# Performance work log

Hardware: AMD Instinct MI355X
Metric: run time of the kernel (lower is better)

The kernel has to match this reference:

```python
import jax, jax.numpy as jnp
import numpy as np

N_NODES = 100000


def gcn_conv(x, W, b, src, dst, num_nodes):
    # PyG GCNConv: add self-loops, symmetric deg^-1/2 normalization,
    # linear transform, scatter-add aggregation at dst, then bias.
    loop = jnp.arange(num_nodes, dtype=src.dtype)
    row = jnp.concatenate([src, loop])  # message sources
    col = jnp.concatenate([dst, loop])  # message destinations
    deg = jax.ops.segment_sum(jnp.ones_like(col, dtype=x.dtype), col,
                              num_segments=num_nodes)
    dinv = jnp.where(deg > 0, jax.lax.rsqrt(deg), 0.0)
    norm = dinv[row] * dinv[col]  # [E+N]
    h = x @ W  # [N, out]
    msg = h[row] * norm[:, None]  # gather + scale, [E+N, out]
    out = jax.ops.segment_sum(msg, col, num_segments=num_nodes)  # scatter-add
    return out + b


def setup_inputs() -> dict:
    key = jax.random.key(0)
    k1, k2, k3, k4, k5, k6 = jax.random.split(key, 6)
    dim_in, dim_h = 256, 128
    E = 1600000
    x = jax.random.normal(k1, (N_NODES, dim_in), dtype=jnp.float32)
    edge_index = jax.random.randint(k2, (2, E), 0, N_NODES, dtype=jnp.int64)
    # Glorot-style init for GCNConv weights
    W1 = jax.random.normal(k3, (dim_in, dim_h), dtype=jnp.float32) * (1.0 / np.sqrt(dim_in))
    b1 = jnp.zeros((dim_h,), dtype=jnp.float32)
    W2 = jax.random.normal(k4, (dim_h, 1), dtype=jnp.float32) * (1.0 / np.sqrt(dim_h))
    b2 = jnp.zeros((1,), dtype=jnp.float32)
    return {"x": x, "edge_index": edge_index, "W1": W1, "b1": b1, "W2": W2, "b2": b2}


def reference(x, edge_index, W1, b1, W2, b2):
    src, dst = edge_index[0], edge_index[1]
    h = gcn_conv(x, W1, b1, src, dst, N_NODES)
    h = jax.nn.relu(h)
    h = gcn_conv(h, W2, b2, src, dst, N_NODES)
    return jax.nn.sigmoid(h)  # [N, 1]
```

## Files before the change

kernel.cpp:

```cpp
#include <hip/hip_runtime.h>
#include <math.h>

#define NN 100000
#define DIN 256
#define DH 128
#define GEMM_NB 1563
#define BSHIFT 9
#define BNODES 512
#define NB_BUCKET 196
#define BCAP 12288
#define PA_EDGES 8192
#define PREP_NB 64

using short8  = __attribute__((ext_vector_type(8))) short;
using float4v = __attribute__((ext_vector_type(4))) float;

static __device__ __forceinline__ unsigned short f2bf(float f) {
    unsigned u = __float_as_uint(f);
    unsigned r = u + 0x7fffu + ((u >> 16) & 1u);
    return (unsigned short)(r >> 16);
}
static __device__ __forceinline__ float bf_lo(unsigned u) { return __uint_as_float(u << 16); }
static __device__ __forceinline__ float bf_hi(unsigned u) { return __uint_as_float(u & 0xffff0000u); }

__global__ __launch_bounds__(512) void k_prep_partA(const float* __restrict__ W1,
                                                    unsigned short* __restrict__ W1p,
                                                    const int* __restrict__ src,
                                                    const int* __restrict__ dst, int E,
                                                    int* __restrict__ bucketFill,
                                                    int2* __restrict__ bucketArr) {
    __shared__ int aCnt[NB_BUCKET];
    __shared__ int aBase[NB_BUCKET];
    const int tid = threadIdx.x;

    if (blockIdx.x < PREP_NB) {
        int t = blockIdx.x * 512 + tid;
        int lane = t & 63;
        int ks   = (t >> 6) & 7;
        int nt   = (t >> 9) & 1;
        int wv   = (t >> 10) & 3;
        int n = wv * 32 + nt * 16 + (lane & 15);
        int kbase = ks * 32 + (lane >> 4) * 8;
        short8 v;
#pragma unroll
        for (int j = 0; j < 8; ++j) v[j] = (short)f2bf(W1[(kbase + j) * DH + n]);
        *(short8*)&W1p[(long long)t * 8] = v;
        return;
    }

    const int ba = blockIdx.x - PREP_NB;
    for (int i = tid; i < NB_BUCKET; i += 512) aCnt[i] = 0;
    __syncthreads();
    const int e0   = ba * PA_EDGES;
    const int eend = min(e0 + PA_EDGES, E);
    for (int e = e0 + tid; e < eend; e += 512)
        atomicAdd(&aCnt[dst[e] >> BSHIFT], 1);
    __syncthreads();
    for (int i = tid; i < NB_BUCKET; i += 512) {
        int c = aCnt[i];
        aBase[i] = c ? atomicAdd(&bucketFill[i], c) : 0;
        aCnt[i] = 0;
    }
    __syncthreads();
    for (int e = e0 + tid; e < eend; e += 512) {
        int d = dst[e];
        int b = d >> BSHIFT;
        int r = atomicAdd(&aCnt[b], 1);
        bucketArr[(long long)b * BCAP + aBase[b] + r] = make_int2(src[e], d);
    }
}

__global__ __launch_bounds__(512) void k_gemm_partB(const float* __restrict__ x,
                                                    const unsigned short* __restrict__ W1p,
                                                    unsigned short* __restrict__ hs,
                                                    const int* __restrict__ bucketFill,
                                                    const int2* __restrict__ bucketArr,
                                                    int* __restrict__ cnt,
                                                    int* __restrict__ excl,
                                                    float* __restrict__ dinv,
                                                    int* __restrict__ eidx) {
    __shared__ unsigned short aL[64 * 32 * 8];
    __shared__ int h[BNODES];
    __shared__ int hex[BNODES];
    __shared__ int st[256];
    const int tid = threadIdx.x;

    if (blockIdx.x < NB_BUCKET) {
        const int b     = blockIdx.x;
        const int nbase = b << BSHIFT;
        const int len   = bucketFill[b];
        const long long abase = (long long)b * BCAP;

        if (tid < 256) st[tid] = (tid < b) ? bucketFill[tid] : 0;
        __syncthreads();
        for (int off = 128; off > 0; off >>= 1) {
            if (tid < off) st[tid] += st[tid + off];
            __syncthreads();
        }
        const int gbase = st[0];
        __syncthreads();

        for (int i = tid; i < BNODES; i += 512) h[i] = 0;
        __syncthreads();
        for (int k = tid; k < len; k += 512)
            atomicAdd(&h[bucketArr[abase + k].y - nbase], 1);
        __syncthreads();

        int a0 = 0, a1 = 0;
        if (tid < 256) {
            a0 = h[2 * tid]; a1 = h[2 * tid + 1];
            st[tid] = a0 + a1;
        }
        __syncthreads();
        for (int off = 1; off < 256; off <<= 1) {
            int val = (tid < 256 && tid >= off) ? st[tid - off] : 0;
            __syncthreads();
            if (tid < 256) st[tid] += val;
            __syncthreads();
        }
        if (tid < 256) {
            int prev = (tid > 0) ? st[tid - 1] : 0;
            hex[2 * tid]     = prev;
            hex[2 * tid + 1] = prev + a0;
        }
        __syncthreads();

        for (int i = tid; i < BNODES; i += 512) {
            int n = nbase + i;
            if (n < NN) {
                int c = h[i];
                cnt[n]  = c;
                excl[n] = gbase + hex[i];
                dinv[n] = rsqrtf(1.0f + (float)c);
            }
        }
        for (int i = tid; i < BNODES; i += 512) h[i] = 0;
        __syncthreads();

        for (int k = tid; k < len; k += 512) {
            int2 p = bucketArr[abase + k];
            int li = p.y - nbase;
            int r = atomicAdd(&h[li], 1);
            eidx[gbase + hex[li] + r] = p.x;
        }
        return;
    }

    const int bid  = blockIdx.x - NB_BUCKET;
    const int w8   = tid >> 6;
    const int lane = tid & 63;
    const int quad = lane >> 4;
    const int m16  = lane & 15;
    const int row0 = bid * 64;

    short8 bfr[8];
#pragma unroll
    for (int ks = 0; ks < 8; ++ks)
        bfr[ks] = ((const short8*)W1p)[(w8 * 8 + ks) * 64 + lane];

#pragma unroll
    for (int it = 0; it < 4; ++it) {
        int id  = it * 512 + tid;
        int row = id >> 5;
        int kb  = id & 31;
        int gr  = row0 + row;
        float4 f0, f1;
        if (gr < NN) {
            const float* xp = &x[(long long)gr * DIN + kb * 8];
            f0 = *(const float4*)xp;
            f1 = *(const float4*)(xp + 4);
        } else {
            f0 = make_float4(0.f, 0.f, 0.f, 0.f);
            f1 = f0;
        }
        short8 v;
        v[0] = (short)f2bf(f0.x); v[1] = (short)f2bf(f0.y);
        v[2] = (short)f2bf(f0.z); v[3] = (short)f2bf(f0.w);
        v[4] = (short)f2bf(f1.x); v[5] = (short)f2bf(f1.y);
        v[6] = (short)f2bf(f1.z); v[7] = (short)f2bf(f1.w);
        int chunk = row * 32 + (kb ^ (row & 31));
        *(short8*)&aL[chunk * 8] = v;
    }
    __syncthreads();

    float4v acc[4];
#pragma unroll
    for (int mt = 0; mt < 4; ++mt) acc[mt] = (float4v)(0.0f);

#pragma unroll
    for (int mt = 0; mt < 4; ++mt) {
        int row = mt * 16 + m16;
#pragma unroll
        for (int ks = 0; ks < 8; ++ks) {
            int kb = ks * 4 + quad;
            int chunk = row * 32 + (kb ^ (row & 31));
            short8 a = *(const short8*)&aL[chunk * 8];
            acc[mt] = __builtin_amdgcn_mfma_f32_16x16x32_bf16(a, bfr[ks], acc[mt], 0, 0, 0);
        }
    }

    const int n0 = w8 * 16;
#pragma unroll
    for (int mt = 0; mt < 4; ++mt) {
#pragma unroll
        for (int r = 0; r < 4; ++r) {
            int row = row0 + mt * 16 + quad * 4 + r;
            if (row < NN)
                hs[(long long)row * DH + n0 + m16] = f2bf(acc[mt][r]);
        }
    }
}

__global__ __launch_bounds__(256) void k_agg1l2(const int* __restrict__ eidx,
                                                const int* __restrict__ excl,
                                                const int* __restrict__ cnt,
                                                const unsigned* __restrict__ hs2,
                                                const float* __restrict__ dinv,
                                                const float* __restrict__ b1,
                                                const float* __restrict__ W2,
                                                float* __restrict__ zs) {
    int w = (blockIdx.x * 256 + threadIdx.x) >> 6;
    if (w >= NN) return;
    const int lane = threadIdx.x & 63;
    const int hh   = lane >> 5;
    const int l5   = lane & 31;
    int offs = excl[w];
    int c    = cnt[w];

    float dw = dinv[w];
    const uint2* hrow = (const uint2*)hs2;

    uint2 su = hrow[(long long)w * 32 + l5];
    float ss = hh ? 0.0f : dw;
    float a0 = ss * bf_lo(su.x);
    float a1 = ss * bf_hi(su.x);
    float a2 = ss * bf_lo(su.y);
    float a3 = ss * bf_hi(su.y);

    int j = 0;
    for (; j + 7 < c; j += 8) {
        int s[4]; float es[4]; uint2 uu[4];
#pragma unroll
        for (int q = 0; q < 4; ++q) s[q] = eidx[offs + j + 2 * q + hh];
#pragma unroll
        for (int q = 0; q < 4; ++q) es[q] = dinv[s[q]];
#pragma unroll
        for (int q = 0; q < 4; ++q) uu[q] = hrow[(long long)s[q] * 32 + l5];
#pragma unroll
        for (int q = 0; q < 4; ++q) {
            a0 = fmaf(es[q], bf_lo(uu[q].x), a0);
            a1 = fmaf(es[q], bf_hi(uu[q].x), a1);
            a2 = fmaf(es[q], bf_lo(uu[q].y), a2);
            a3 = fmaf(es[q], bf_hi(uu[q].y), a3);
        }
    }
    for (; j + 1 < c; j += 2) {
        int s0 = eidx[offs + j + hh];
        float e0 = dinv[s0];
        uint2 u0 = hrow[(long long)s0 * 32 + l5];
        a0 = fmaf(e0, bf_lo(u0.x), a0);
        a1 = fmaf(e0, bf_hi(u0.x), a1);
        a2 = fmaf(e0, bf_lo(u0.y), a2);
        a3 = fmaf(e0, bf_hi(u0.y), a3);
    }
    if (j < c) {
        int s0 = eidx[offs + j];
        float e0 = hh ? 0.0f : dinv[s0];
        uint2 u0 = hrow[(long long)s0 * 32 + l5];
        a0 = fmaf(e0, bf_lo(u0.x), a0);
        a1 = fmaf(e0, bf_hi(u0.x), a1);
        a2 = fmaf(e0, bf_lo(u0.y), a2);
        a3 = fmaf(e0, bf_hi(u0.y), a3);
    }

    a0 += __shfl_xor(a0, 32);
    a1 += __shfl_xor(a1, 32);
    a2 += __shfl_xor(a2, 32);
    a3 += __shfl_xor(a3, 32);

    float4 bb = ((const float4*)b1)[l5];
    float4 ww = ((const float4*)W2)[l5];
    float r0 = fmaxf(fmaf(dw, a0, bb.x), 0.0f);
    float r1 = fmaxf(fmaf(dw, a1, bb.y), 0.0f);
    float r2 = fmaxf(fmaf(dw, a2, bb.z), 0.0f);
    float r3 = fmaxf(fmaf(dw, a3, bb.w), 0.0f);
    float v = r0 * ww.x + r1 * ww.y + r2 * ww.z + r3 * ww.w;
#pragma unroll
    for (int off = 16; off > 0; off >>= 1) v += __shfl_down(v, off);
    if (lane == 0) zs[w] = v * dw;
}

__global__ void k_agg2_final(const int* __restrict__ eidx,
                             const int* __restrict__ excl,
                             const int* __restrict__ cnt,
                             const float* __restrict__ zs,
                             const float* __restrict__ dinv,
                             const float* __restrict__ b2,
                             float* __restrict__ out) {
    int i = blockIdx.x * 256 + threadIdx.x;
    if (i >= NN) return;
    int offs = excl[i];
    int c = cnt[i];
    float v = zs[i];
    int j = 0;
    for (; j + 3 < c; j += 4) {
        int s0 = eidx[offs + j + 0];
        int s1 = eidx[offs + j + 1];
        int s2 = eidx[offs + j + 2];
        int s3 = eidx[offs + j + 3];
        v += zs[s0] + zs[s1] + zs[s2] + zs[s3];
    }
    for (; j < c; ++j) v += zs[eidx[offs + j]];
    float z = fmaf(dinv[i], v, b2[0]);
    out[i] = 1.0f / (1.0f + __expf(-z));
}

extern "C" void kernel_launch(void* const* d_in, const int* in_sizes, int n_in,
                              void* d_out, int out_size, void* d_ws, size_t ws_size,
                              hipStream_t stream) {
    const float* x  = (const float*)d_in[0];
    const int*   ei = (const int*)d_in[1];
    const float* W1 = (const float*)d_in[2];
    const float* b1 = (const float*)d_in[3];
    const float* W2 = (const float*)d_in[4];
    const float* b2 = (const float*)d_in[5];
    float* out = (float*)d_out;

    const int E = in_sizes[1] / 2;
    const int* src = ei;
    const int* dst = ei + E;

    int* wsi = (int*)d_ws;
    float* dinv       = (float*)wsi;
    int*   cnt        = wsi + NN;
    int*   excl       = cnt + NN;
    float* zs         = (float*)(excl + NN);
    int*   bucketFill = (int*)(zs + NN);
    unsigned short* W1p = (unsigned short*)(bucketFill + 256);
    int*   eidx       = (int*)(W1p + 32768);
    int2*  bucketArr  = (int2*)(eidx + E);
    unsigned short* hs = (unsigned short*)(bucketArr + (long long)NB_BUCKET * BCAP);

    const int nb_nodes = (NN + 255) / 256;
    const int pa_nb = (E + PA_EDGES - 1) / PA_EDGES;

    hipMemsetAsync(bucketFill, 0, NB_BUCKET * sizeof(int), stream);

    k_prep_partA<<<PREP_NB + pa_nb, 512, 0, stream>>>(W1, W1p, src, dst, E,
                                                      bucketFill, bucketArr);
    k_gemm_partB<<<NB_BUCKET + GEMM_NB, 512, 0, stream>>>(x, W1p, hs, bucketFill, bucketArr,
                                                          cnt, excl, dinv, eidx);

    k_agg1l2<<<(NN * 64 + 255) / 256, 256, 0, stream>>>(eidx, excl, cnt,
                                                        (const unsigned*)hs, dinv, b1, W2, zs);

    k_agg2_final<<<nb_nodes, 256, 0, stream>>>(eidx, excl, cnt, zs, dinv, b2, out);
}
```

Measured before the change: 288.2 us.

## Replace bucketed CSR build with global atomic count, scan, and scatter

Drops the two-level bucket sort, which wrote int2 pairs into per-bucket arrays and then re-sorted them locally. CSR is now built from a global atomic degree count, a 4-block prefix scan fused into the GEMM launch, and a separate scatter kernel that uses global atomics on per-node cursors. Nontemporal loads are added for x, dst/src and eidx. The aim is to cut intermediate memory traffic, at the cost of heavy global atomic contention, a serial per-thread scan segment, and one extra kernel launch.

After: 519.9 us. +80.4%, slower.

```diff
diff --git a/kernel.cpp b/kernel.cpp
--- a/kernel.cpp
+++ b/kernel.cpp
@@ -5,12 +5,10 @@
 #define DIN 256
 #define DH 128
 #define GEMM_NB 1563
-#define BSHIFT 9
-#define BNODES 512
-#define NB_BUCKET 196
-#define BCAP 12288
-#define PA_EDGES 8192
 #define PREP_NB 64
+#define CNT_NB 448
+#define SCAN_NB 4
+#define SCAN_CHUNK 25000
 
 using short8  = __attribute__((ext_vector_type(8))) short;
 using float4v = __attribute__((ext_vector_type(4))) float;
@@ -23,14 +21,10 @@
 static __device__ __forceinline__ float bf_lo(unsigned u) { return __uint_as_float(u << 16); }
 static __device__ __forceinline__ float bf_hi(unsigned u) { return __uint_as_float(u & 0xffff0000u); }
 
-__global__ __launch_bounds__(512) void k_prep_partA(const float* __restrict__ W1,
+__global__ __launch_bounds__(512) void k_prep_count(const float* __restrict__ W1,
                                                     unsigned short* __restrict__ W1p,
-                                                    const int* __restrict__ src,
                                                     const int* __restrict__ dst, int E,
-                                                    int* __restrict__ bucketFill,
-                                                    int2* __restrict__ bucketArr) {
-    __shared__ int aCnt[NB_BUCKET];
-    __shared__ int aBase[NB_BUCKET];
+                                                    int* __restrict__ cnt) {
     const int tid = threadIdx.x;
 
     if (blockIdx.x < PREP_NB) {
@@ -48,105 +42,67 @@
         return;
     }
 
-    const int ba = blockIdx.x - PREP_NB;
-    for (int i = tid; i < NB_BUCKET; i += 512) aCnt[i] = 0;
-    __syncthreads();
-    const int e0   = ba * PA_EDGES;
-    const int eend = min(e0 + PA_EDGES, E);
-    for (int e = e0 + tid; e < eend; e += 512)
-        atomicAdd(&aCnt[dst[e] >> BSHIFT], 1);
-    __syncthreads();
-    for (int i = tid; i < NB_BUCKET; i += 512) {
-        int c = aCnt[i];
-        aBase[i] = c ? atomicAdd(&bucketFill[i], c) : 0;
-        aCnt[i] = 0;
-    }
-    __syncthreads();
-    for (int e = e0 + tid; e < eend; e += 512) {
-        int d = dst[e];
-        int b = d >> BSHIFT;
-        int r = atomicAdd(&aCnt[b], 1);
-        bucketArr[(long long)b * BCAP + aBase[b] + r] = make_int2(src[e], d);
-    }
-}
-
-__global__ __launch_bounds__(512) void k_gemm_partB(const float* __restrict__ x,
-                                                    const unsigned short* __restrict__ W1p,
-                                                    unsigned short* __restrict__ hs,
-                                                    const int* __restrict__ bucketFill,
-                                                    const int2* __restrict__ bucketArr,
-                                                    int* __restrict__ cnt,
-                                                    int* __restrict__ excl,
-                                                    float* __restrict__ dinv,
-                                                    int* __restrict__ eidx) {
+    const int stride = CNT_NB * 512;
+    for (int e = (blockIdx.x - PREP_NB) * 512 + tid; e < E; e += stride) {
+        int d = __builtin_nontemporal_load(&dst[e]);
+        atomicAdd(&cnt[d], 1);
+    }
+}
+
+__global__ __launch_bounds__(512) void k_gemm_scan(const float* __restrict__ x,
+                                                   const unsigned short* __restrict__ W1p,
+                                                   unsigned short* __restrict__ hs,
+                                                   const int* __restrict__ cnt,
+                                                   int* __restrict__ excl,
+                                                   int* __restrict__ cur,
+                                                   float* __restrict__ dinv) {
     __shared__ unsigned short aL[64 * 32 * 8];
-    __shared__ int h[BNODES];
-    __shared__ int hex[BNODES];
-    __shared__ int st[256];
     const int tid = threadIdx.x;
 
-    if (blockIdx.x < NB_BUCKET) {
-        const int b     = blockIdx.x;
-        const int nbase = b << BSHIFT;
-        const int len   = bucketFill[b];
-        const long long abase = (long long)b * BCAP;
-
-        if (tid < 256) st[tid] = (tid < b) ? bucketFill[tid] : 0;
+    if (blockIdx.x < SCAN_NB) {
+        int* red = (int*)aL;
+        const int b  = blockIdx.x;
+        const int lo = b * SCAN_CHUNK;
+        const int hi = min(lo + SCAN_CHUNK, NN);
+
+        int part = 0;
+        for (int i = tid; i < lo; i += 512) part += cnt[i];
+        red[tid] = part;
         __syncthreads();
-        for (int off = 128; off > 0; off >>= 1) {
-            if (tid < off) st[tid] += st[tid + off];
+        for (int off = 256; off > 0; off >>= 1) {
+            if (tid < off) red[tid] += red[tid + off];
             __syncthreads();
         }
-        const int gbase = st[0];
+        const int base = red[0];
         __syncthreads();
 
-        for (int i = tid; i < BNODES; i += 512) h[i] = 0;
+        const int CH = (SCAN_CHUNK + 511) / 512;
+        const int t0 = lo + tid * CH;
+        const int t1 = min(t0 + CH, hi);
+        int ts = 0;
+        for (int i = t0; i < t1; ++i) ts += cnt[i];
+
+        red[tid] = ts;
         __syncthreads();
-        for (int k = tid; k < len; k += 512)
-            atomicAdd(&h[bucketArr[abase + k].y - nbase], 1);
-        __syncthreads();
-
-        int a0 = 0, a1 = 0;
-        if (tid < 256) {
-            a0 = h[2 * tid]; a1 = h[2 * tid + 1];
-            st[tid] = a0 + a1;
-        }
-        __syncthreads();
-        for (int off = 1; off < 256; off <<= 1) {
-            int val = (tid < 256 && tid >= off) ? st[tid - off] : 0;
+        for (int off = 1; off < 512; off <<= 1) {
+            int v = (tid >= off) ? red[tid - off] : 0;
             __syncthreads();
-            if (tid < 256) st[tid] += val;
+            red[tid] += v;
             __syncthreads();
         }
-        if (tid < 256) {
-            int prev = (tid > 0) ? st[tid - 1] : 0;
-            hex[2 * tid]     = prev;
-            hex[2 * tid + 1] = prev + a0;
-        }
-        __syncthreads();
-
-        for (int i = tid; i < BNODES; i += 512) {
-            int n = nbase + i;
-            if (n < NN) {
-                int c = h[i];
-                cnt[n]  = c;
-                excl[n] = gbase + hex[i];
-                dinv[n] = rsqrtf(1.0f + (float)c);
-            }
-        }
-        for (int i = tid; i < BNODES; i += 512) h[i] = 0;
-        __syncthreads();
-
-        for (int k = tid; k < len; k += 512) {
-            int2 p = bucketArr[abase + k];
-            int li = p.y - nbase;
-            int r = atomicAdd(&h[li], 1);
-            eidx[gbase + hex[li] + r] = p.x;
+        int run = base + (tid ? red[tid - 1] : 0);
+
+        for (int i = t0; i < t1; ++i) {
+            int c = cnt[i];
+            excl[i] = run;
+            cur[i]  = run;
+            dinv[i] = rsqrtf(1.0f + (float)c);
+            run += c;
         }
         return;
     }
 
-    const int bid  = blockIdx.x - NB_BUCKET;
+    const int bid  = blockIdx.x - SCAN_NB;
     const int w8   = tid >> 6;
     const int lane = tid & 63;
     const int quad = lane >> 4;
@@ -164,20 +120,20 @@
         int row = id >> 5;
         int kb  = id & 31;
         int gr  = row0 + row;
-        float4 f0, f1;
+        float4v f0, f1;
         if (gr < NN) {
-            const float* xp = &x[(long long)gr * DIN + kb * 8];
-            f0 = *(const float4*)xp;
-            f1 = *(const float4*)(xp + 4);
+            const float4v* xp = (const float4v*)&x[(long long)gr * DIN + kb * 8];
+            f0 = __builtin_nontemporal_load(xp);
+            f1 = __builtin_nontemporal_load(xp + 1);
         } else {
-            f0 = make_float4(0.f, 0.f, 0.f, 0.f);
-            f1 = f0;
+            f0 = (float4v)(0.0f);
+            f1 = (float4v)(0.0f);
         }
         short8 v;
-        v[0] = (short)f2bf(f0.x); v[1] = (short)f2bf(f0.y);
-        v[2] = (short)f2bf(f0.z); v[3] = (short)f2bf(f0.w);
-        v[4] = (short)f2bf(f1.x); v[5] = (short)f2bf(f1.y);
-        v[6] = (short)f2bf(f1.z); v[7] = (short)f2bf(f1.w);
+        v[0] = (short)f2bf(f0[0]); v[1] = (short)f2bf(f0[1]);
+        v[2] = (short)f2bf(f0[2]); v[3] = (short)f2bf(f0[3]);
+        v[4] = (short)f2bf(f1[0]); v[5] = (short)f2bf(f1[1]);
+        v[6] = (short)f2bf(f1[2]); v[7] = (short)f2bf(f1[3]);
         int chunk = row * 32 + (kb ^ (row & 31));
         *(short8*)&aL[chunk * 8] = v;
     }
@@ -208,6 +164,19 @@
             if (row < NN)
                 hs[(long long)row * DH + n0 + m16] = f2bf(acc[mt][r]);
         }
+    }
+}
+
+__global__ __launch_bounds__(256) void k_scatter(const int* __restrict__ src,
+                                                 const int* __restrict__ dst, int E,
+                                                 int* __restrict__ cur,
+                                                 int* __restrict__ eidx) {
+    const int stride = gridDim.x * 256;
+    for (int e = blockIdx.x * 256 + threadIdx.x; e < E; e += stride) {
+        int d = __builtin_nontemporal_load(&dst[e]);
+        int s = __builtin_nontemporal_load(&src[e]);
+        int p = atomicAdd(&cur[d], 1);
+        eidx[p] = s;
     }
 }
 
@@ -304,10 +273,10 @@
     float v = zs[i];
     int j = 0;
     for (; j + 3 < c; j += 4) {
-        int s0 = eidx[offs + j + 0];
-        int s1 = eidx[offs + j + 1];
-        int s2 = eidx[offs + j + 2];
-        int s3 = eidx[offs + j + 3];
+        int s0 = __builtin_nontemporal_load(&eidx[offs + j + 0]);
+        int s1 = __builtin_nontemporal_load(&eidx[offs + j + 1]);
+        int s2 = __builtin_nontemporal_load(&eidx[offs + j + 2]);
+        int s3 = __builtin_nontemporal_load(&eidx[offs + j + 3]);
         v += zs[s0] + zs[s1] + zs[s2] + zs[s3];
     }
     for (; j < c; ++j) v += zs[eidx[offs + j]];
@@ -334,25 +303,20 @@
     float* dinv       = (float*)wsi;
     int*   cnt        = wsi + NN;
     int*   excl       = cnt + NN;
-    float* zs         = (float*)(excl + NN);
-    int*   bucketFill = (int*)(zs + NN);
-    unsigned short* W1p = (unsigned short*)(bucketFill + 256);
+    int*   cur        = excl + NN;
+    float* zs         = (float*)(cur + NN);
+    unsigned short* W1p = (unsigned short*)(zs + NN);
     int*   eidx       = (int*)(W1p + 32768);
-    int2*  bucketArr  = (int2*)(eidx + E);
-    unsigned short* hs = (unsigned short*)(bucketArr + (long long)NB_BUCKET * BCAP);
+    unsigned short* hs = (unsigned short*)(eidx + E + (E & 1));
 
     const int nb_nodes = (NN + 255) / 256;
-    const int pa_nb = (E + PA_EDGES - 1) / PA_EDGES;
-
-    hipMemsetAsync(bucketFill, 0, NB_BUCKET * sizeof(int), stream);
-
-    k_prep_partA<<<PREP_NB + pa_nb, 512, 0, stream>>>(W1, W1p, src, dst, E,
-                                                      bucketFill, bucketArr);
-    k_gemm_partB<<<NB_BUCKET + GEMM_NB, 512, 0, stream>>>(x, W1p, hs, bucketFill, bucketArr,
-                                                          cnt, excl, dinv, eidx);
-
+
+    hipMemsetAsync(cnt, 0, NN * sizeof(int), stream);
+
+    k_prep_count<<<PREP_NB + CNT_NB, 512, 0, stream>>>(W1, W1p, dst, E, cnt);
+    k_gemm_scan<<<SCAN_NB + GEMM_NB, 512, 0, stream>>>(x, W1p, hs, cnt, excl, cur, dinv);
+    k_scatter<<<2048, 256, 0, stream>>>(src, dst, E, cur, eidx);
     k_agg1l2<<<(NN * 64 + 255) / 256, 256, 0, stream>>>(eidx, excl, cnt,
                                                         (const unsigned*)hs, dinv, b1, W2, zs);
-
     k_agg2_final<<<nb_nodes, 256, 0, stream>>>(eidx, excl, cnt, zs, dinv, b2, out);
 }
```
